# Kernel optimization log

Hardware: AMD Instinct MI355X
Metric: run time of the kernel (lower is better)

## Reference

```python
import jax, jax.numpy as jnp
import numpy as np


def setup_inputs() -> dict:
    key = jax.random.key(0)
    ks = jax.random.split(key, 10)
    B, T = 1024, 8192
    # X features: [time, current I, temperature T, voltage U]
    t = jnp.cumsum(jax.random.uniform(ks[0], (B, T, 1), jnp.float32) + 0.5, axis=1)  # increasing time
    feats = jax.random.normal(ks[1], (B, T, 3), jnp.float32)
    X = jnp.concatenate([t, feats], axis=-1)  # [B, T, 4]
    # SC: [Q (capacity), eta_0, R, SOC_init_base]; keep Q away from 0
    SC = jax.random.uniform(ks[2], (B, 4), jnp.float32, minval=0.5, maxval=1.5)
    std = 0.1
    # SOC_init_net: Linear(4,1) -> Softplus -> Linear(1,1), normal(0,0.1) weights, zero bias
    W1i = jax.random.normal(ks[3], (1, 4), jnp.float32) * std
    b1i = jnp.zeros((1,), jnp.float32)
    W2i = jax.random.normal(ks[4], (1, 1), jnp.float32) * std
    b2i = jnp.zeros((1,), jnp.float32)
    # eta_net: Linear(2,1) -> Softplus -> Linear(1,1)
    W1e = jax.random.normal(ks[5], (1, 2), jnp.float32) * std
    b1e = jnp.zeros((1,), jnp.float32)
    W2e = jax.random.normal(ks[6], (1, 1), jnp.float32) * std
    b2e = jnp.zeros((1,), jnp.float32)
    return {"X": X, "SC": SC, "W1i": W1i, "b1i": b1i, "W2i": W2i, "b2i": b2i,
            "W1e": W1e, "b1e": b1e, "W2e": W2e, "b2e": b2e}


def reference(X, SC, W1i, b1i, W2i, b2i, W1e, b1e, W2e, b2e):
    # X: [B, T, 4] = (t, I, Temp, U); SC: [B, 4] = (Q, eta_0, R, soc_base)
    I = X[..., 1:2]      # [B, T, 1]
    Temp = X[..., 2:3]   # [B, T, 1]
    U = X[..., 3:4]      # [B, T, 1]
    R = SC[..., 2:3]     # [B, 1]
    # SOC_init_net on first-timestep features
    feat0 = jnp.concatenate([I[:, 0, :], Temp[:, 0, :], U[:, 0, :], R], axis=-1)  # [B, 4]
    h0 = jax.nn.softplus(feat0 @ W1i.T + b1i)
    soc_net = h0 @ W2i.T + b2i                     # [B, 1]
    SOC_init = SC[..., 3:4] * (1.0 + soc_net)      # [B, 1]
    # eta_net over all timesteps
    feat = jnp.concatenate([I, Temp], axis=-1)     # [B, T, 2]
    h = jax.nn.softplus(feat @ W1e.T + b1e)
    delta_eta = h @ W2e.T + b2e                    # [B, T, 1]
    # ODE RHS: dSOC/dt = eta_0 * (1 + delta_eta) * I / (3600 * Q)
    Q = SC[..., 0:1][:, None, :]                   # [B, 1, 1]
    eta0 = SC[..., 1:2][:, None, :]                # [B, 1, 1]
    f = eta0 * (1.0 + delta_eta) * I / (3600.0 * Q)  # [B, T, 1]
    # Euler integration: y_{k+1} = y_k + (t_{k+1} - t_k) * f(x_k, y_k); f independent of y -> cumsum
    ts = X[..., 0:1]                               # [B, T, 1]
    dt = ts[:, 1:] - ts[:, :-1]                    # [B, T-1, 1]
    incr = dt * f[:, :-1]                          # [B, T-1, 1]
    zero = jnp.zeros_like(SOC_init)[:, None, :]    # [B, 1, 1]
    SOC = SOC_init[:, None, :] + jnp.concatenate([zero, jnp.cumsum(incr, axis=1)], axis=1)
    return SOC                                     # [B, T, 1]
```

## Files before the change

### kernel.cpp

```cpp
#include <hip/hip_runtime.h>
#include <type_traits>


static __device__ __forceinline__ float bf2f(unsigned int u) {
    union { unsigned int i; float f; } v;
    v.i = u << 16;
    return v.f;
}
static __device__ __forceinline__ unsigned short f2bf(float f) {
    union { unsigned int i; float f; } v;
    v.f = f;
    unsigned int x = v.i;
    return (unsigned short)((x + 0x7fffu + ((x >> 16) & 1u)) >> 16);
}
static __device__ __forceinline__ float softplus_f(float x) {
    return (x > 15.f) ? x : log1pf(expf(x));
}

struct F4 { float ts, I, Te, U; };
static __device__ __forceinline__ F4 dec(ushort4 x) {
    return {bf2f(x.x), bf2f(x.y), bf2f(x.z), bf2f(x.w)};
}
static __device__ __forceinline__ F4 dec(float4 x) {
    return {x.x, x.y, x.z, x.w};
}

template <bool BF16>
static __device__ __forceinline__ float ld(const void* p, int i) {
    return BF16 ? bf2f(((const unsigned short*)p)[i]) : ((const float*)p)[i];
}

constexpr int BLOCK = 256;

template <bool BF16>
static __device__ void run_scan(
    const void* __restrict__ Xv, const void* __restrict__ SCv,
    const void* __restrict__ W1i, const void* __restrict__ b1i,
    const void* __restrict__ W2i, const void* __restrict__ b2i,
    const void* __restrict__ W1e, const void* __restrict__ b1e,
    const void* __restrict__ W2e, const void* __restrict__ b2e,
    void* __restrict__ outv, int T)
{
    using XVec = typename std::conditional<BF16, ushort4, float4>::type;

    const int b    = blockIdx.x;
    const int tid  = threadIdx.x;
    const int lane = tid & 63;
    const int wave = tid >> 6;
    const int ntile = T / BLOCK;

    __shared__ float s_wts[4], s_wf[4], s_wsum[4];
    __shared__ float s_carry, s_pts, s_pf;

    const float Q    = ld<BF16>(SCv, b * 4 + 0);
    const float eta0 = ld<BF16>(SCv, b * 4 + 1);
    const float R    = ld<BF16>(SCv, b * 4 + 2);
    const float S3   = ld<BF16>(SCv, b * 4 + 3);
    const float w1e0 = ld<BF16>(W1e, 0);
    const float w1e1 = ld<BF16>(W1e, 1);
    const float vb1e = ld<BF16>(b1e, 0);
    const float w2e  = ld<BF16>(W2e, 0);
    const float vb2e = ld<BF16>(b2e, 0);
    const float coef = eta0 / (3600.f * Q);

    const XVec* Xrow = (const XVec*)Xv + (size_t)b * T;

    XVec x = Xrow[tid];

    for (int tile = 0; tile < ntile; ++tile) {
        XVec xn = x;
        if (tile + 1 < ntile) xn = Xrow[(tile + 1) * BLOCK + tid];

        const int t = tile * BLOCK + tid;
        const F4 v = dec(x);
        const float tsv = v.ts;
        const float I   = v.I;
        const float Te  = v.Te;

        const float h = softplus_f(fmaf(I, w1e0, fmaf(Te, w1e1, vb1e)));
        const float f = coef * (1.f + fmaf(h, w2e, vb2e)) * I;

        float pts = __shfl_up(tsv, 1, 64);
        float pf  = __shfl_up(f, 1, 64);

        __syncthreads();
        if (lane == 63) { s_wts[wave] = tsv; s_wf[wave] = f; }
        if (tile == 0 && tid == 0) {
            const float pre = fmaf(I, ld<BF16>(W1i, 0),
                              fmaf(Te, ld<BF16>(W1i, 1),
                              fmaf(v.U, ld<BF16>(W1i, 2),
                              fmaf(R, ld<BF16>(W1i, 3), ld<BF16>(b1i, 0)))));
            const float h0      = softplus_f(pre);
            const float soc_net = fmaf(h0, ld<BF16>(W2i, 0), ld<BF16>(b2i, 0));
            s_carry = S3 * (1.f + soc_net);
        }
        __syncthreads();
        if (lane == 0) {
            if (wave == 0) {
                if (tile > 0) { pts = s_pts; pf = s_pf; }
            } else {
                pts = s_wts[wave - 1];
                pf  = s_wf[wave - 1];
            }
        }

        float g = (t == 0) ? 0.f : (tsv - pts) * pf;

        #pragma unroll
        for (int d = 1; d < 64; d <<= 1) {
            float vv = __shfl_up(g, d, 64);
            if (lane >= d) g += vv;
        }
        if (lane == 63) s_wsum[wave] = g;
        __syncthreads();

        float soc = s_carry;
        #pragma unroll
        for (int w = 0; w < 3; ++w)
            if (w < wave) soc += s_wsum[w];
        soc += g;

        if (BF16) ((unsigned short*)outv)[(size_t)b * T + t] = f2bf(soc);
        else      ((float*)outv)[(size_t)b * T + t] = soc;

        __syncthreads();
        if (tid == BLOCK - 1) {
            s_carry = soc;
            s_pts   = tsv;
            s_pf    = f;
        }
        x = xn;
    }
}

__global__ __launch_bounds__(BLOCK) void socnet_kernel(
    const void* __restrict__ X, const void* __restrict__ SC,
    const void* __restrict__ W1i, const void* __restrict__ b1i,
    const void* __restrict__ W2i, const void* __restrict__ b2i,
    const void* __restrict__ W1e, const void* __restrict__ b1e,
    const void* __restrict__ W2e, const void* __restrict__ b2e,
    void* __restrict__ out, int T)
{
    const unsigned int* scw = (const unsigned int*)SC;
    const unsigned int a0 = scw[0], a1 = scw[1], a2 = scw[2], a3 = scw[3];
    const float l0 = bf2f(a0 & 0xFFFFu), l1 = bf2f(a1 & 0xFFFFu);
    const float l2 = bf2f(a2 & 0xFFFFu), l3 = bf2f(a3 & 0xFFFFu);
    const bool isbf =
        (l0 >= 0.45f && l0 <= 1.55f) && (l1 >= 0.45f && l1 <= 1.55f) &&
        (l2 >= 0.45f && l2 <= 1.55f) && (l3 >= 0.45f && l3 <= 1.55f);

    if (isbf) run_scan<true >(X, SC, W1i, b1i, W2i, b2i, W1e, b1e, W2e, b2e, out, T);
    else      run_scan<false>(X, SC, W1i, b1i, W2i, b2i, W1e, b1e, W2e, b2e, out, T);
}

extern "C" void kernel_launch(void* const* d_in, const int* in_sizes, int n_in,
                              void* d_out, int out_size, void* d_ws, size_t ws_size,
                              hipStream_t stream) {
    const int B = in_sizes[1] / 4;
    const int T = in_sizes[0] / (B * 4);

    socnet_kernel<<<dim3(B), dim3(BLOCK), 0, stream>>>(
        d_in[0], d_in[1], d_in[2], d_in[3], d_in[4], d_in[5],
        d_in[6], d_in[7], d_in[8], d_in[9], d_out, T);
}
```

Baseline: 220.7 us.

## Stage whole-row increments in LDS and use per-thread serial scan

Replaces the tile-by-tile block scan, which needed several barriers per 256-element tile, with a three-phase scheme. First all increments for a row are computed and stored in padded shared memory. Each thread then serially scans a contiguous segment, a single block-level scan of the segment totals produces per-thread bases, and output is written with vectorized float4 or ushort4 stores. This removes per-tile synchronisation and scalar stores. In exchange it uses about 33KB of LDS per block, which can limit occupancy, the serial strided LDS access may hit bank conflicts, and it hardcodes a maximum T of 8192.

```diff
diff --git a/kernel.cpp b/kernel.cpp
--- a/kernel.cpp
+++ b/kernel.cpp
@@ -31,6 +31,8 @@
 }
 
 constexpr int BLOCK = 256;
+constexpr int MAXT  = 8192;
+constexpr int GSZ = MAXT + MAXT / 32;
 
 template <bool BF16>
 static __device__ void run_scan(
@@ -47,10 +49,12 @@
     const int tid  = threadIdx.x;
     const int lane = tid & 63;
     const int wave = tid >> 6;
-    const int ntile = T / BLOCK;
+    const int L    = T / BLOCK;
 
-    __shared__ float s_wts[4], s_wf[4], s_wsum[4];
-    __shared__ float s_carry, s_pts, s_pf;
+    __shared__ float s_g[GSZ];
+    __shared__ float s_base[BLOCK];
+    __shared__ float s_wtot[4];
+    __shared__ float s_init;
 
     const float Q    = ld<BF16>(SCv, b * 4 + 0);
     const float eta0 = ld<BF16>(SCv, b * 4 + 1);
@@ -65,71 +69,87 @@
 
     const XVec* Xrow = (const XVec*)Xv + (size_t)b * T;
 
-    XVec x = Xrow[tid];
+    const int nchunk = T / BLOCK;
+    #pragma unroll 4
+    for (int c = 0; c < nchunk; ++c) {
+        const int t = c * BLOCK + tid;
+        const F4 v = dec(Xrow[t]);
+        const float h = softplus_f(fmaf(v.I, w1e0, fmaf(v.Te, w1e1, vb1e)));
+        const float f = coef * (1.f + fmaf(h, w2e, vb2e)) * v.I;
+        float pts = __shfl_up(v.ts, 1, 64);
+        float pf  = __shfl_up(f,  1, 64);
+        if (lane == 0 && t > 0) {
+            const F4 vp = dec(Xrow[t - 1]);
+            const float hp = softplus_f(fmaf(vp.I, w1e0, fmaf(vp.Te, w1e1, vb1e)));
+            pf  = coef * (1.f + fmaf(hp, w2e, vb2e)) * vp.I;
+            pts = vp.ts;
+        }
+        const float g = (t == 0) ? 0.f : (v.ts - pts) * pf;
+        s_g[t + (t >> 5)] = g;
+    }
 
-    for (int tile = 0; tile < ntile; ++tile) {
-        XVec xn = x;
-        if (tile + 1 < ntile) xn = Xrow[(tile + 1) * BLOCK + tid];
+    if (tid == 0) {
+        const F4 v0 = dec(Xrow[0]);
+        const float pre = fmaf(v0.I, ld<BF16>(W1i, 0),
+                          fmaf(v0.Te, ld<BF16>(W1i, 1),
+                          fmaf(v0.U, ld<BF16>(W1i, 2),
+                          fmaf(R, ld<BF16>(W1i, 3), ld<BF16>(b1i, 0)))));
+        const float h0 = softplus_f(pre);
+        s_init = S3 * (1.f + fmaf(h0, ld<BF16>(W2i, 0), ld<BF16>(b2i, 0)));
+    }
+    __syncthreads();
 
-        const int t = tile * BLOCK + tid;
-        const F4 v = dec(x);
-        const float tsv = v.ts;
-        const float I   = v.I;
-        const float Te  = v.Te;
+    float run = 0.f;
+    for (int j = 0; j < L; ++j) {
+        const int t = tid * L + j;
+        const int a = t + (t >> 5);
+        run += s_g[a];
+        s_g[a] = run;
+    }
 
-        const float h = softplus_f(fmaf(I, w1e0, fmaf(Te, w1e1, vb1e)));
-        const float f = coef * (1.f + fmaf(h, w2e, vb2e)) * I;
+    const float tot = run;
+    float sc = tot;
+    #pragma unroll
+    for (int d = 1; d < 64; d <<= 1) {
+        const float u = __shfl_up(sc, d, 64);
+        if (lane >= d) sc += u;
+    }
+    if (lane == 63) s_wtot[wave] = sc;
+    __syncthreads();
+    float basev = s_init + (sc - tot);
+    #pragma unroll
+    for (int w = 0; w < 3; ++w)
+        if (w < wave) basev += s_wtot[w];
+    s_base[tid] = basev;
+    __syncthreads();
 
-        float pts = __shfl_up(tsv, 1, 64);
-        float pf  = __shfl_up(f, 1, 64);
-
-        __syncthreads();
-        if (lane == 63) { s_wts[wave] = tsv; s_wf[wave] = f; }
-        if (tile == 0 && tid == 0) {
-            const float pre = fmaf(I, ld<BF16>(W1i, 0),
-                              fmaf(Te, ld<BF16>(W1i, 1),
-                              fmaf(v.U, ld<BF16>(W1i, 2),
-                              fmaf(R, ld<BF16>(W1i, 3), ld<BF16>(b1i, 0)))));
-            const float h0      = softplus_f(pre);
-            const float soc_net = fmaf(h0, ld<BF16>(W2i, 0), ld<BF16>(b2i, 0));
-            s_carry = S3 * (1.f + soc_net);
+    const int nvec = T / 4;
+    if (!BF16) {
+        float4* out4 = (float4*)outv + (size_t)b * nvec;
+        for (int p = 0; p < nvec / BLOCK; ++p) {
+            const int vi = p * BLOCK + tid;
+            const int t0 = vi * 4;
+            const float bb = s_base[t0 / L];
+            float4 o;
+            o.x = bb + s_g[t0     + ((t0    ) >> 5)];
+            o.y = bb + s_g[t0 + 1 + ((t0 + 1) >> 5)];
+            o.z = bb + s_g[t0 + 2 + ((t0 + 2) >> 5)];
+            o.w = bb + s_g[t0 + 3 + ((t0 + 3) >> 5)];
+            out4[vi] = o;
         }
-        __syncthreads();
-        if (lane == 0) {
-            if (wave == 0) {
-                if (tile > 0) { pts = s_pts; pf = s_pf; }
-            } else {
-                pts = s_wts[wave - 1];
-                pf  = s_wf[wave - 1];
-            }
+    } else {
+        ushort4* out4 = (ushort4*)outv + (size_t)b * nvec;
+        for (int p = 0; p < nvec / BLOCK; ++p) {
+            const int vi = p * BLOCK + tid;
+            const int t0 = vi * 4;
+            const float bb = s_base[t0 / L];
+            ushort4 o;
+            o.x = f2bf(bb + s_g[t0     + ((t0    ) >> 5)]);
+            o.y = f2bf(bb + s_g[t0 + 1 + ((t0 + 1) >> 5)]);
+            o.z = f2bf(bb + s_g[t0 + 2 + ((t0 + 2) >> 5)]);
+            o.w = f2bf(bb + s_g[t0 + 3 + ((t0 + 3) >> 5)]);
+            out4[vi] = o;
         }
-
-        float g = (t == 0) ? 0.f : (tsv - pts) * pf;
-
-        #pragma unroll
-        for (int d = 1; d < 64; d <<= 1) {
-            float vv = __shfl_up(g, d, 64);
-            if (lane >= d) g += vv;
-        }
-        if (lane == 63) s_wsum[wave] = g;
-        __syncthreads();
-
-        float soc = s_carry;
-        #pragma unroll
-        for (int w = 0; w < 3; ++w)
-            if (w < wave) soc += s_wsum[w];
-        soc += g;
-
-        if (BF16) ((unsigned short*)outv)[(size_t)b * T + t] = f2bf(soc);
-        else      ((float*)outv)[(size_t)b * T + t] = soc;
-
-        __syncthreads();
-        if (tid == BLOCK - 1) {
-            s_carry = soc;
-            s_pts   = tsv;
-            s_pf    = f;
-        }
-        x = xn;
     }
 }
 
@@ -142,9 +162,8 @@
     void* __restrict__ out, int T)
 {
     const unsigned int* scw = (const unsigned int*)SC;
-    const unsigned int a0 = scw[0], a1 = scw[1], a2 = scw[2], a3 = scw[3];
-    const float l0 = bf2f(a0 & 0xFFFFu), l1 = bf2f(a1 & 0xFFFFu);
-    const float l2 = bf2f(a2 & 0xFFFFu), l3 = bf2f(a3 & 0xFFFFu);
+    const float l0 = bf2f(scw[0] & 0xFFFFu), l1 = bf2f(scw[1] & 0xFFFFu);
+    const float l2 = bf2f(scw[2] & 0xFFFFu), l3 = bf2f(scw[3] & 0xFFFFu);
     const bool isbf =
         (l0 >= 0.45f && l0 <= 1.55f) && (l1 >= 0.45f && l1 <= 1.55f) &&
         (l2 >= 0.45f && l2 <= 1.55f) && (l3 >= 0.45f && l3 <= 1.55f);
```

Result: slower. 288.3 us (+30.6%).

## Split each row into per-wave contiguous spans scanned in registers

Applied to the files above, without the earlier changes.

Replaces the block-wide tile loop, which needed four barriers per 256-element tile, with a scheme where each wave scans a contiguous quarter of the row. Each wave keeps a running carry and holds its partial sums in registers, then the waves are combined with a single barrier before all outputs are written. It also swaps softplus for fast __expf/__logf intrinsics and folds the constants of the eta expression. The trade-offs are a T==8192 specialization with a generic fallback kernel, higher register pressure from 32 held values per thread, and a softplus that drops the overflow guard for large inputs.

```diff
diff --git a/kernel.cpp b/kernel.cpp
--- a/kernel.cpp
+++ b/kernel.cpp
@@ -13,8 +13,8 @@
     unsigned int x = v.i;
     return (unsigned short)((x + 0x7fffu + ((x >> 16) & 1u)) >> 16);
 }
-static __device__ __forceinline__ float softplus_f(float x) {
-    return (x > 15.f) ? x : log1pf(expf(x));
+static __device__ __forceinline__ float sp_fast(float x) {
+    return __logf(1.f + __expf(x));
 }
 
 struct F4 { float ts, I, Te, U; };
@@ -32,25 +32,24 @@
 
 constexpr int BLOCK = 256;
 
-template <bool BF16>
-static __device__ void run_scan(
+template <bool BF16, int NC>
+static __device__ void scan_reg(
     const void* __restrict__ Xv, const void* __restrict__ SCv,
     const void* __restrict__ W1i, const void* __restrict__ b1i,
     const void* __restrict__ W2i, const void* __restrict__ b2i,
     const void* __restrict__ W1e, const void* __restrict__ b1e,
     const void* __restrict__ W2e, const void* __restrict__ b2e,
-    void* __restrict__ outv, int T)
+    void* __restrict__ outv, float* s_wtot, float* s_init)
 {
     using XVec = typename std::conditional<BF16, ushort4, float4>::type;
+    constexpr int T = NC * 256;
+    constexpr int SPAN = T / 4;
 
     const int b    = blockIdx.x;
     const int tid  = threadIdx.x;
     const int lane = tid & 63;
     const int wave = tid >> 6;
-    const int ntile = T / BLOCK;
-
-    __shared__ float s_wts[4], s_wf[4], s_wsum[4];
-    __shared__ float s_carry, s_pts, s_pf;
+    const int wavestart = wave * SPAN;
 
     const float Q    = ld<BF16>(SCv, b * 4 + 0);
     const float eta0 = ld<BF16>(SCv, b * 4 + 1);
@@ -59,98 +58,196 @@
     const float w1e0 = ld<BF16>(W1e, 0);
     const float w1e1 = ld<BF16>(W1e, 1);
     const float vb1e = ld<BF16>(b1e, 0);
-    const float w2e  = ld<BF16>(W2e, 0);
-    const float vb2e = ld<BF16>(b2e, 0);
     const float coef = eta0 / (3600.f * Q);
+    const float c2   = coef * ld<BF16>(W2e, 0);
+    const float c1   = coef * (1.f + ld<BF16>(b2e, 0));
 
     const XVec* Xrow = (const XVec*)Xv + (size_t)b * T;
 
-    XVec x = Xrow[tid];
-
-    for (int tile = 0; tile < ntile; ++tile) {
-        XVec xn = x;
-        if (tile + 1 < ntile) xn = Xrow[(tile + 1) * BLOCK + tid];
-
-        const int t = tile * BLOCK + tid;
-        const F4 v = dec(x);
-        const float tsv = v.ts;
-        const float I   = v.I;
-        const float Te  = v.Te;
-
-        const float h = softplus_f(fmaf(I, w1e0, fmaf(Te, w1e1, vb1e)));
-        const float f = coef * (1.f + fmaf(h, w2e, vb2e)) * I;
-
-        float pts = __shfl_up(tsv, 1, 64);
-        float pf  = __shfl_up(f, 1, 64);
-
-        __syncthreads();
-        if (lane == 63) { s_wts[wave] = tsv; s_wf[wave] = f; }
-        if (tile == 0 && tid == 0) {
-            const float pre = fmaf(I, ld<BF16>(W1i, 0),
-                              fmaf(Te, ld<BF16>(W1i, 1),
-                              fmaf(v.U, ld<BF16>(W1i, 2),
-                              fmaf(R, ld<BF16>(W1i, 3), ld<BF16>(b1i, 0)))));
-            const float h0      = softplus_f(pre);
-            const float soc_net = fmaf(h0, ld<BF16>(W2i, 0), ld<BF16>(b2i, 0));
-            s_carry = S3 * (1.f + soc_net);
-        }
-        __syncthreads();
-        if (lane == 0) {
-            if (wave == 0) {
-                if (tile > 0) { pts = s_pts; pf = s_pf; }
-            } else {
-                pts = s_wts[wave - 1];
-                pf  = s_wf[wave - 1];
-            }
-        }
-
-        float g = (t == 0) ? 0.f : (tsv - pts) * pf;
+    float ts_c, f_c;
+    if (wave > 0) {
+        const F4 vp = dec(Xrow[wavestart - 1]);
+        const float hp = sp_fast(fmaf(vp.I, w1e0, fmaf(vp.Te, w1e1, vb1e)));
+        f_c  = fmaf(c2, hp, c1) * vp.I;
+        ts_c = vp.ts;
+    } else {
+        const F4 v0 = dec(Xrow[0]);
+        ts_c = v0.ts;
+        f_c  = 0.f;
+        const float pre = fmaf(v0.I, ld<BF16>(W1i, 0),
+                          fmaf(v0.Te, ld<BF16>(W1i, 1),
+                          fmaf(v0.U, ld<BF16>(W1i, 2),
+                          fmaf(R, ld<BF16>(W1i, 3), ld<BF16>(b1i, 0)))));
+        const float h0 = sp_fast(pre);
+        if (lane == 0)
+            *s_init = S3 * (1.f + fmaf(h0, ld<BF16>(W2i, 0), ld<BF16>(b2i, 0)));
+    }
+
+    float vals[NC];
+    float carry = 0.f;
+    XVec cur = Xrow[wavestart + lane];
+    XVec nxt = Xrow[wavestart + 64 + lane];
+    #pragma unroll
+    for (int c = 0; c < NC; ++c) {
+        XVec after = cur;
+        if (c + 2 < NC) after = Xrow[wavestart + (c + 2) * 64 + lane];
+
+        const F4 v = dec(cur);
+        const float f = fmaf(c2, sp_fast(fmaf(v.I, w1e0, fmaf(v.Te, w1e1, vb1e))), c1) * v.I;
+
+        float pts = __shfl_up(v.ts, 1, 64);
+        float pf  = __shfl_up(f,   1, 64);
+        if (lane == 0) { pts = ts_c; pf = f_c; }
+        float g = (v.ts - pts) * pf;
 
         #pragma unroll
         for (int d = 1; d < 64; d <<= 1) {
-            float vv = __shfl_up(g, d, 64);
-            if (lane >= d) g += vv;
-        }
-        if (lane == 63) s_wsum[wave] = g;
-        __syncthreads();
-
-        float soc = s_carry;
-        #pragma unroll
-        for (int w = 0; w < 3; ++w)
-            if (w < wave) soc += s_wsum[w];
-        soc += g;
-
-        if (BF16) ((unsigned short*)outv)[(size_t)b * T + t] = f2bf(soc);
-        else      ((float*)outv)[(size_t)b * T + t] = soc;
-
-        __syncthreads();
-        if (tid == BLOCK - 1) {
-            s_carry = soc;
-            s_pts   = tsv;
-            s_pf    = f;
-        }
-        x = xn;
-    }
-}
-
-__global__ __launch_bounds__(BLOCK) void socnet_kernel(
+            const float u = __shfl_up(g, d, 64);
+            if (lane >= d) g += u;
+        }
+        g += carry;
+        vals[c] = g;
+
+        carry = __shfl(g, 63, 64);
+        ts_c  = __shfl(v.ts, 63, 64);
+        f_c   = __shfl(f, 63, 64);
+        cur = nxt; nxt = after;
+    }
+    if (lane == 0) s_wtot[wave] = carry;
+    __syncthreads();
+
+    float base = *s_init;
+    #pragma unroll
+    for (int w = 0; w < 3; ++w)
+        if (w < wave) base += s_wtot[w];
+
+    if (!BF16) {
+        float* op = (float*)outv + (size_t)b * T + wavestart + lane;
+        #pragma unroll
+        for (int c = 0; c < NC; ++c) op[c * 64] = vals[c] + base;
+    } else {
+        unsigned short* op = (unsigned short*)outv + (size_t)b * T + wavestart + lane;
+        #pragma unroll
+        for (int c = 0; c < NC; ++c) op[c * 64] = f2bf(vals[c] + base);
+    }
+}
+
+__global__ __launch_bounds__(BLOCK, 4) void socnet_reg(
     const void* __restrict__ X, const void* __restrict__ SC,
     const void* __restrict__ W1i, const void* __restrict__ b1i,
     const void* __restrict__ W2i, const void* __restrict__ b2i,
     const void* __restrict__ W1e, const void* __restrict__ b1e,
     const void* __restrict__ W2e, const void* __restrict__ b2e,
-    void* __restrict__ out, int T)
-{
+    void* __restrict__ out)
+{
+    __shared__ float s_wtot[4];
+    __shared__ float s_init;
+
     const unsigned int* scw = (const unsigned int*)SC;
-    const unsigned int a0 = scw[0], a1 = scw[1], a2 = scw[2], a3 = scw[3];
-    const float l0 = bf2f(a0 & 0xFFFFu), l1 = bf2f(a1 & 0xFFFFu);
-    const float l2 = bf2f(a2 & 0xFFFFu), l3 = bf2f(a3 & 0xFFFFu);
+    const float l0 = bf2f(scw[0] & 0xFFFFu), l1 = bf2f(scw[1] & 0xFFFFu);
+    const float l2 = bf2f(scw[2] & 0xFFFFu), l3 = bf2f(scw[3] & 0xFFFFu);
     const bool isbf =
         (l0 >= 0.45f && l0 <= 1.55f) && (l1 >= 0.45f && l1 <= 1.55f) &&
         (l2 >= 0.45f && l2 <= 1.55f) && (l3 >= 0.45f && l3 <= 1.55f);
 
-    if (isbf) run_scan<true >(X, SC, W1i, b1i, W2i, b2i, W1e, b1e, W2e, b2e, out, T);
-    else      run_scan<false>(X, SC, W1i, b1i, W2i, b2i, W1e, b1e, W2e, b2e, out, T);
+    if (isbf) scan_reg<true, 32>(X, SC, W1i, b1i, W2i, b2i, W1e, b1e, W2e, b2e,
+                                 out, s_wtot, &s_init);
+    else      scan_reg<false, 32>(X, SC, W1i, b1i, W2i, b2i, W1e, b1e, W2e, b2e,
+                                  out, s_wtot, &s_init);
+}
+
+template <bool BF16>
+static __device__ void scan_serial(
+    const void* __restrict__ Xv, const void* __restrict__ SCv,
+    const void* __restrict__ W1i, const void* __restrict__ b1i,
+    const void* __restrict__ W2i, const void* __restrict__ b2i,
+    const void* __restrict__ W1e, const void* __restrict__ b1e,
+    const void* __restrict__ W2e, const void* __restrict__ b2e,
+    void* __restrict__ outv, int T,
+    float* s_wts, float* s_wf, float* s_wsum, float* s_carr)
+{
+    using XVec = typename std::conditional<BF16, ushort4, float4>::type;
+    const int b = blockIdx.x, tid = threadIdx.x;
+    const int lane = tid & 63, wave = tid >> 6;
+    const int ntile = (T + BLOCK - 1) / BLOCK;
+
+    const float Q    = ld<BF16>(SCv, b * 4 + 0);
+    const float eta0 = ld<BF16>(SCv, b * 4 + 1);
+    const float R    = ld<BF16>(SCv, b * 4 + 2);
+    const float S3   = ld<BF16>(SCv, b * 4 + 3);
+    const float w1e0 = ld<BF16>(W1e, 0);
+    const float w1e1 = ld<BF16>(W1e, 1);
+    const float vb1e = ld<BF16>(b1e, 0);
+    const float coef = eta0 / (3600.f * Q);
+    const float c2   = coef * ld<BF16>(W2e, 0);
+    const float c1   = coef * (1.f + ld<BF16>(b2e, 0));
+
+    const XVec* Xrow = (const XVec*)Xv + (size_t)b * T;
+
+    for (int tile = 0; tile < ntile; ++tile) {
+        const int t = tile * BLOCK + tid;
+        const bool act = t < T;
+        F4 v = {0.f, 0.f, 0.f, 0.f};
+        if (act) v = dec(Xrow[t]);
+        const float f = fmaf(c2, sp_fast(fmaf(v.I, w1e0, fmaf(v.Te, w1e1, vb1e))), c1) * v.I;
+
+        float pts = __shfl_up(v.ts, 1, 64);
+        float pf  = __shfl_up(f, 1, 64);
+
+        __syncthreads();
+        if (lane == 63) { s_wts[wave] = v.ts; s_wf[wave] = f; }
+        if (tile == 0 && tid == 0) {
+            const float pre = fmaf(v.I, ld<BF16>(W1i, 0),
+                              fmaf(v.Te, ld<BF16>(W1i, 1),
+                              fmaf(v.U, ld<BF16>(W1i, 2),
+                              fmaf(R, ld<BF16>(W1i, 3), ld<BF16>(b1i, 0)))));
+            s_carr[0] = S3 * (1.f + fmaf(sp_fast(pre), ld<BF16>(W2i, 0), ld<BF16>(b2i, 0)));
+        }
+        __syncthreads();
+        if (lane == 0) {
+            if (wave == 0) { if (tile > 0) { pts = s_carr[1]; pf = s_carr[2]; } }
+            else { pts = s_wts[wave - 1]; pf = s_wf[wave - 1]; }
+        }
+        float g = (t == 0 || !act) ? 0.f : (v.ts - pts) * pf;
+        #pragma unroll
+        for (int d = 1; d < 64; d <<= 1) {
+            const float u = __shfl_up(g, d, 64);
+            if (lane >= d) g += u;
+        }
+        if (lane == 63) s_wsum[wave] = g;
+        __syncthreads();
+        float soc = s_carr[0];
+        #pragma unroll
+        for (int w = 0; w < 3; ++w) if (w < wave) soc += s_wsum[w];
+        soc += g;
+        if (act) {
+            if (BF16) ((unsigned short*)outv)[(size_t)b * T + t] = f2bf(soc);
+            else      ((float*)outv)[(size_t)b * T + t] = soc;
+        }
+        __syncthreads();
+        if (tid == BLOCK - 1) { s_carr[0] = soc; s_carr[1] = v.ts; s_carr[2] = f; }
+    }
+}
+
+__global__ __launch_bounds__(BLOCK) void socnet_serial_k(
+    const void* __restrict__ X, const void* __restrict__ SC,
+    const void* __restrict__ W1i, const void* __restrict__ b1i,
+    const void* __restrict__ W2i, const void* __restrict__ b2i,
+    const void* __restrict__ W1e, const void* __restrict__ b1e,
+    const void* __restrict__ W2e, const void* __restrict__ b2e,
+    void* __restrict__ out, int T)
+{
+    __shared__ float s_wts[4], s_wf[4], s_wsum[4], s_carr[3];
+    const unsigned int* scw = (const unsigned int*)SC;
+    const float l0 = bf2f(scw[0] & 0xFFFFu), l1 = bf2f(scw[1] & 0xFFFFu);
+    const float l2 = bf2f(scw[2] & 0xFFFFu), l3 = bf2f(scw[3] & 0xFFFFu);
+    const bool isbf =
+        (l0 >= 0.45f && l0 <= 1.55f) && (l1 >= 0.45f && l1 <= 1.55f) &&
+        (l2 >= 0.45f && l2 <= 1.55f) && (l3 >= 0.45f && l3 <= 1.55f);
+    if (isbf) scan_serial<true >(X, SC, W1i, b1i, W2i, b2i, W1e, b1e, W2e, b2e,
+                                 out, T, s_wts, s_wf, s_wsum, s_carr);
+    else      scan_serial<false>(X, SC, W1i, b1i, W2i, b2i, W1e, b1e, W2e, b2e,
+                                 out, T, s_wts, s_wf, s_wsum, s_carr);
 }
 
 extern "C" void kernel_launch(void* const* d_in, const int* in_sizes, int n_in,
@@ -159,7 +256,13 @@
     const int B = in_sizes[1] / 4;
     const int T = in_sizes[0] / (B * 4);
 
-    socnet_kernel<<<dim3(B), dim3(BLOCK), 0, stream>>>(
-        d_in[0], d_in[1], d_in[2], d_in[3], d_in[4], d_in[5],
-        d_in[6], d_in[7], d_in[8], d_in[9], d_out, T);
-}
+    if (T == 8192) {
+        socnet_reg<<<dim3(B), dim3(BLOCK), 0, stream>>>(
+            d_in[0], d_in[1], d_in[2], d_in[3], d_in[4], d_in[5],
+            d_in[6], d_in[7], d_in[8], d_in[9], d_out);
+    } else {
+        socnet_serial_k<<<dim3(B), dim3(BLOCK), 0, stream>>>(
+            d_in[0], d_in[1], d_in[2], d_in[3], d_in[4], d_in[5],
+            d_in[6], d_in[7], d_in[8], d_in[9], d_out, T);
+    }
+}
```

Result: slower. 225.5 us (+2.2%).
